# Kernel tuning notes

Hardware: AMD Instinct MI355X
Metric: run time of the kernel (lower is better)

Reference implementation:

```python
import jax, jax.numpy as jnp
import numpy as np
from jax import lax

DIM = 192
WS = (8, 8)
HEADS = 6
N = WS[0] * WS[1]
HEAD_DIM = DIM // HEADS
SCALE = HEAD_DIM ** -0.5


def _relative_position_index():
    ch, cw = np.arange(WS[0]), np.arange(WS[1])
    coords = np.stack(np.meshgrid(ch, cw, indexing='ij'))  # (2, Wh, Ww)
    cf = coords.reshape(2, -1)                              # (2, N)
    rel = cf[:, :, None] - cf[:, None, :]                   # (2, N, N)
    rel = rel.transpose(1, 2, 0).copy()
    rel[:, :, 0] += WS[0] - 1
    rel[:, :, 1] += WS[1] - 1
    rel[:, :, 0] *= 2 * WS[1] - 1
    return rel.sum(-1).astype(np.int32)                     # (N, N)


def setup_inputs() -> dict:
    key = jax.random.key(0)
    ks = jax.random.split(key, 8)
    B_ = 2048
    C3 = 3 * DIM
    x = jax.random.normal(ks[0], (B_, N, DIM), dtype=jnp.float32)
    mask = jnp.zeros((64, N, N), dtype=jnp.float32)  # (nW, N, N), 0/-inf mask; zeros here
    qkv_w = jax.random.normal(ks[1], (C3, DIM), dtype=jnp.float32) * 0.02   # 1x1 conv weight
    qkv_b = jnp.zeros((C3,), dtype=jnp.float32)
    dw_w = jax.random.normal(ks[2], (C3, 1, 3, 3), dtype=jnp.float32) * 0.1  # depthwise OIHW
    dw_b = jnp.zeros((C3,), dtype=jnp.float32)
    rpb_table = jax.random.normal(ks[3], ((2 * WS[0] - 1) * (2 * WS[1] - 1), HEADS), dtype=jnp.float32) * 0.02
    rel_idx = jnp.asarray(_relative_position_index())
    proj_w = jax.random.normal(ks[4], (DIM, DIM), dtype=jnp.float32) * 0.02
    proj_b = jnp.zeros((DIM,), dtype=jnp.float32)
    return {"x": x, "mask": mask, "qkv_w": qkv_w, "qkv_b": qkv_b, "dw_w": dw_w,
            "dw_b": dw_b, "rpb_table": rpb_table, "rel_idx": rel_idx,
            "proj_w": proj_w, "proj_b": proj_b}


def reference(x, mask, qkv_w, qkv_b, dw_w, dw_b, rpb_table, rel_idx, proj_w, proj_b):
    B_, n, C = x.shape
    C3 = 3 * C
    # 1x1 conv over channel dim (input treated as unbatched (C, B_, N) image)
    t = jnp.einsum('bnc,oc->bno', x, qkv_w) + qkv_b            # (B_, N, 3C)
    # depthwise 3x3 conv over the (B_, N) "spatial" grid, per the torch code
    t4 = t.transpose(2, 0, 1)[None]                            # (1, 3C, B_, N)
    t4 = lax.conv_general_dilated(
        t4, dw_w, window_strides=(1, 1), padding='SAME',
        feature_group_count=C3,
        dimension_numbers=('NCHW', 'OIHW', 'NCHW'))
    temp = (t4[0] + dw_b[:, None, None]).transpose(1, 2, 0)    # (B_, N, 3C)
    qkv = temp.reshape(B_, n, 3, HEADS, HEAD_DIM).transpose(2, 0, 3, 1, 4)
    q, k, v = qkv[0] * SCALE, qkv[1], qkv[2]                   # (B_, H, N, d)
    attn = jnp.einsum('bhnd,bhmd->bhnm', q, k)                 # (B_, H, N, N)
    bias = rpb_table[rel_idx.reshape(-1)].reshape(n, n, HEADS).transpose(2, 0, 1)
    attn = attn + bias[None]
    nW = mask.shape[0]
    attn = attn.reshape(B_ // nW, nW, HEADS, n, n) + mask[None, :, None]
    attn = jax.nn.softmax(attn.reshape(B_, HEADS, n, n), axis=-1)
    out = jnp.einsum('bhnm,bhmd->bhnd', attn, v)               # (B_, H, N, d)
    out = out.transpose(0, 2, 1, 3).reshape(B_, n, C)
    return out @ proj_w.T + proj_b
```

## Files before the change

kernel.cpp:

```cpp
#include <hip/hip_runtime.h>

#define NWIN 2048
#define NPOS 64
#define DIM  192
#define C3   576
#define HEADS 6
#define HD   32
#define MTOT (NWIN*NPOS)
#define SCALE 0.17677669529663687f

typedef __bf16 b16x8 __attribute__((ext_vector_type(8)));
typedef __bf16 b16x4 __attribute__((ext_vector_type(4)));
typedef float  f32x4 __attribute__((ext_vector_type(4)));

__device__ __forceinline__ b16x8 ld8(const float* p) {
    const f32x4 f0 = *(const f32x4*)p;
    const f32x4 f1 = *(const f32x4*)(p + 4);
    b16x8 r;
    r[0] = (__bf16)f0[0]; r[1] = (__bf16)f0[1]; r[2] = (__bf16)f0[2]; r[3] = (__bf16)f0[3];
    r[4] = (__bf16)f1[0]; r[5] = (__bf16)f1[1]; r[6] = (__bf16)f1[2]; r[7] = (__bf16)f1[3];
    return r;
}
__device__ __forceinline__ b16x8 ld8(const __bf16* p) { return *(const b16x8*)p; }

#define GTM 128
#define GTN 64
#define GLD 72

template <typename TA, typename TC>
__global__ __launch_bounds__(256, 3)
void gemm_bt(const TA* __restrict__ A, const float* __restrict__ W,
             const float* __restrict__ bias, TC* __restrict__ C, int N)
{
    __shared__ __bf16 As[GTM][GLD];
    __shared__ __bf16 Ws[GTN][GLD];
    const int ntiles = N / GTN;
    const int cpx = gridDim.x >> 3;
    const int lb  = (blockIdx.x & 7) * cpx + (blockIdx.x >> 3);
    const int bm = lb / ntiles;
    const int bn = lb % ntiles;
    const long m0 = (long)bm * GTM;
    const int  n0 = bn * GTN;
    const int tid  = threadIdx.x;
    const int wave = tid >> 6, lane = tid & 63;
    const int lr = lane & 15, lq = lane >> 4;

    f32x4 acc[2][4];
#pragma unroll
    for (int i = 0; i < 2; i++)
#pragma unroll
        for (int j = 0; j < 4; j++) acc[i][j] = (f32x4){0.f, 0.f, 0.f, 0.f};

    for (int kc = 0; kc < 3; kc++) {
#pragma unroll
        for (int i = 0; i < 4; i++) {
            int idx = tid + i * 256;
            int r = idx >> 3, c = idx & 7;
            *(b16x8*)&As[r][c * 8] = ld8(A + (m0 + r) * 192 + kc * 64 + c * 8);
        }
#pragma unroll
        for (int i = 0; i < 2; i++) {
            int idx = tid + i * 256;
            int r = idx >> 3, c = idx & 7;
            *(b16x8*)&Ws[r][c * 8] = ld8(W + (long)(n0 + r) * 192 + kc * 64 + c * 8);
        }
        __syncthreads();
#pragma unroll
        for (int kt = 0; kt < 2; kt++) {
            const int k0 = kt * 32 + lq * 8;
            b16x8 a0 = *(const b16x8*)&As[wave * 32 + lr][k0];
            b16x8 a1 = *(const b16x8*)&As[wave * 32 + 16 + lr][k0];
            b16x8 b0 = *(const b16x8*)&Ws[lr][k0];
            b16x8 b1 = *(const b16x8*)&Ws[16 + lr][k0];
            b16x8 b2 = *(const b16x8*)&Ws[32 + lr][k0];
            b16x8 b3 = *(const b16x8*)&Ws[48 + lr][k0];
            acc[0][0] = __builtin_amdgcn_mfma_f32_16x16x32_bf16(a0, b0, acc[0][0], 0, 0, 0);
            acc[0][1] = __builtin_amdgcn_mfma_f32_16x16x32_bf16(a0, b1, acc[0][1], 0, 0, 0);
            acc[0][2] = __builtin_amdgcn_mfma_f32_16x16x32_bf16(a0, b2, acc[0][2], 0, 0, 0);
            acc[0][3] = __builtin_amdgcn_mfma_f32_16x16x32_bf16(a0, b3, acc[0][3], 0, 0, 0);
            acc[1][0] = __builtin_amdgcn_mfma_f32_16x16x32_bf16(a1, b0, acc[1][0], 0, 0, 0);
            acc[1][1] = __builtin_amdgcn_mfma_f32_16x16x32_bf16(a1, b1, acc[1][1], 0, 0, 0);
            acc[1][2] = __builtin_amdgcn_mfma_f32_16x16x32_bf16(a1, b2, acc[1][2], 0, 0, 0);
            acc[1][3] = __builtin_amdgcn_mfma_f32_16x16x32_bf16(a1, b3, acc[1][3], 0, 0, 0);
        }
        __syncthreads();
    }
#pragma unroll
    for (int tn = 0; tn < 4; tn++) {
        float bv = bias[n0 + tn * 16 + lr];
#pragma unroll
        for (int tm = 0; tm < 2; tm++) {
#pragma unroll
            for (int r = 0; r < 4; r++) {
                long row = m0 + wave * 32 + tm * 16 + lq * 4 + r;
                C[row * N + (n0 + tn * 16 + lr)] = (TC)(acc[tm][tn][r] + bv);
            }
        }
    }
}

__global__ __launch_bounds__(576)
void dwconv(const __bf16* __restrict__ t, const float* __restrict__ dw_w,
            const float* __restrict__ dw_b, __bf16* __restrict__ u)
{
    const int tid = threadIdx.x;
    const int cg  = tid % 144;
    const int mr  = tid / 144;
    const int c0  = cg * 4;

    float w[9][4], bias[4];
#pragma unroll
    for (int e = 0; e < 4; e++) {
        bias[e] = dw_b[c0 + e];
#pragma unroll
        for (int tp = 0; tp < 9; tp++) w[tp][e] = dw_w[(c0 + e) * 9 + tp];
    }
    const float sc = (c0 < DIM) ? SCALE : 1.0f;

    const int b = blockIdx.x;
    const bool up = (b > 0), dn = (b < NWIN - 1);
    const __bf16* tb = t + (long)b * NPOS * C3 + c0;
    __bf16*       ub = u + (long)b * NPOS * C3 + c0;

    for (int i = 0; i < 16; i++) {
        const int n = i * 4 + mr;
        float acc[4] = {bias[0], bias[1], bias[2], bias[3]};
#pragma unroll
        for (int kh = 0; kh < 3; kh++) {
            if ((kh == 0 && !up) || (kh == 2 && !dn)) continue;
            const __bf16* rp = tb + (long)(kh - 1) * NPOS * C3 + (long)n * C3;
#pragma unroll
            for (int kw = 0; kw < 3; kw++) {
                const int nn = n + kw - 1;
                if (nn < 0 || nn >= NPOS) continue;
                b16x4 v = *(const b16x4*)(rp + (kw - 1) * C3);
#pragma unroll
                for (int e = 0; e < 4; e++) acc[e] += (float)v[e] * w[kh * 3 + kw][e];
            }
        }
        b16x4 o;
#pragma unroll
        for (int e = 0; e < 4; e++) o[e] = (__bf16)(acc[e] * sc);
        *(b16x4*)(ub + (long)n * C3) = o;
    }
}

#define P0v2 0
#define VT0  4608

__global__ __launch_bounds__(64, 3)
void attn_mfma(const __bf16* __restrict__ u, const float* __restrict__ mask,
               const float* __restrict__ rpb, __bf16* __restrict__ ctx)
{
    __shared__ __bf16 smem[4608 + 2304];
    __shared__ float  rpb_h[225];
    const int cpx = gridDim.x >> 3;
    const int lb  = (blockIdx.x & 7) * cpx + (blockIdx.x >> 3);
    const int b = lb / HEADS;
    const int h = lb % HEADS;
    const int lane = threadIdx.x;
    const int lr = lane & 15, lq = lane >> 4;

    for (int i = lane; i < 225; i += 64) rpb_h[i] = rpb[i * HEADS + h];

    const __bf16* ub = u + (long)b * NPOS * C3 + h * HD;

    {
        const __bf16* vp = ub + (long)lane * C3 + 2 * DIM;
        b16x8 v0 = *(const b16x8*)vp;
        b16x8 v1 = *(const b16x8*)(vp + 8);
        b16x8 v2 = *(const b16x8*)(vp + 16);
        b16x8 v3 = *(const b16x8*)(vp + 24);
#pragma unroll
        for (int e = 0; e < 8; e++) {
            smem[VT0 + (e     ) * 72 + lane] = v0[e];
            smem[VT0 + (e +  8) * 72 + lane] = v1[e];
            smem[VT0 + (e + 16) * 72 + lane] = v2[e];
            smem[VT0 + (e + 24) * 72 + lane] = v3[e];
        }
    }

    b16x8 aq[4], bk[4];
#pragma unroll
    for (int t4 = 0; t4 < 4; t4++) {
        aq[t4] = *(const b16x8*)(ub + (long)(t4 * 16 + lr) * C3 +       lq * 8);
        bk[t4] = *(const b16x8*)(ub + (long)(t4 * 16 + lr) * C3 + DIM + lq * 8);
    }

    f32x4 S[4][4];
#pragma unroll
    for (int tm = 0; tm < 4; tm++)
#pragma unroll
        for (int tn = 0; tn < 4; tn++) {
            S[tm][tn] = (f32x4){0.f, 0.f, 0.f, 0.f};
            S[tm][tn] = __builtin_amdgcn_mfma_f32_16x16x32_bf16(aq[tm], bk[tn], S[tm][tn], 0, 0, 0);
        }

    __syncthreads();

    const float* mbase = mask + (long)(b & 63) * 4096;
    float part[4][4];
#pragma unroll
    for (int tm = 0; tm < 4; tm++)
#pragma unroll
        for (int r = 0; r < 4; r++) part[tm][r] = 0.f;
#pragma unroll
    for (int tm = 0; tm < 4; tm++) {
#pragma unroll
        for (int r = 0; r < 4; r++) {
            const int row = tm * 16 + lq * 4 + r;
            const int rh = row >> 3, rw = row & 7;
#pragma unroll
            for (int tn = 0; tn < 4; tn++) {
                const int col = tn * 16 + lr;
                const int ridx = (rh - (col >> 3) + 7) * 15 + (rw - (col & 7) + 7);
                float sv = S[tm][tn][r] + rpb_h[ridx] + mbase[row * 64 + col];
                float ee = __expf(sv);
                part[tm][r] += ee;
                smem[P0v2 + row * 72 + col] = (__bf16)ee;
            }
        }
    }
#pragma unroll
    for (int st = 1; st < 16; st <<= 1)
#pragma unroll
        for (int tm = 0; tm < 4; tm++)
#pragma unroll
            for (int r = 0; r < 4; r++) part[tm][r] += __shfl_xor(part[tm][r], st);
    float inv[4][4];
#pragma unroll
    for (int tm = 0; tm < 4; tm++)
#pragma unroll
        for (int r = 0; r < 4; r++) inv[tm][r] = 1.0f / part[tm][r];

    __syncthreads();

    f32x4 O[4][2];
#pragma unroll
    for (int tm = 0; tm < 4; tm++)
#pragma unroll
        for (int tn2 = 0; tn2 < 2; tn2++) O[tm][tn2] = (f32x4){0.f, 0.f, 0.f, 0.f};
#pragma unroll
    for (int tk = 0; tk < 2; tk++) {
        b16x8 bv[2];
#pragma unroll
        for (int tn2 = 0; tn2 < 2; tn2++)
            bv[tn2] = *(const b16x8*)&smem[VT0 + (tn2 * 16 + lr) * 72 + tk * 32 + lq * 8];
#pragma unroll
        for (int tm = 0; tm < 4; tm++) {
            b16x8 ap = *(const b16x8*)&smem[P0v2 + (tm * 16 + lr) * 72 + tk * 32 + lq * 8];
#pragma unroll
            for (int tn2 = 0; tn2 < 2; tn2++)
                O[tm][tn2] = __builtin_amdgcn_mfma_f32_16x16x32_bf16(ap, bv[tn2], O[tm][tn2], 0, 0, 0);
        }
    }

#pragma unroll
    for (int tm = 0; tm < 4; tm++)
#pragma unroll
        for (int tn2 = 0; tn2 < 2; tn2++)
#pragma unroll
            for (int r = 0; r < 4; r++) {
                const int row = tm * 16 + lq * 4 + r;
                ctx[(long)(b * NPOS + row) * DIM + h * HD + tn2 * 16 + lr] =
                    (__bf16)(O[tm][tn2][r] * inv[tm][r]);
            }
}

#define Q0 0
#define K0 2560
#define P0 0
#define V0 5120

__global__ __launch_bounds__(64, 4)
void attn_fused(const __bf16* __restrict__ t, const float* __restrict__ dw_w,
                const float* __restrict__ dw_b, const float* __restrict__ mask,
                const float* __restrict__ rpb, __bf16* __restrict__ ctx)
{
    __shared__ __bf16 smem[7424];
    __shared__ float  rpb_h[225];
    const int bid = blockIdx.x;
    const int h   = bid >> 11;
    const int s_  = bid & 2047;
    const int b   = (s_ & 7) * 256 + (s_ >> 3);
    const int lane = threadIdx.x;
    const int lr = lane & 15, lq = lane >> 4;

    for (int i = lane; i < 225; i += 64) rpb_h[i] = rpb[i * HEADS + h];

    {
        const int kv = lane >> 5, d = lane & 31;
        const int o  = 192 + kv * 192 + h * 32 + d;
        float w[9];
#pragma unroll
        for (int tap = 0; tap < 9; tap++) w[tap] = dw_w[o * 9 + tap];
        const float cb = dw_b[o];
        const bool up = (b > 0), dn = (b < NWIN - 1);
        const __bf16* r1 = t + (long)b * NPOS * C3 + o;
        const __bf16* r0 = r1 - (long)NPOS * C3;
        const __bf16* r2 = r1 + (long)NPOS * C3;
        float p0 = 0.f, c0 = up ? (float)r0[0] : 0.f;
        float p1 = 0.f, c1 = (float)r1[0];
        float p2 = 0.f, c2 = dn ? (float)r2[0] : 0.f;
        const int base = kv ? (V0 + d * 72) : (K0 + d);
        const int step = kv ? 1 : 40;
        for (int nn = 0; nn < 64; nn++) {
            float n0 = 0.f, n1 = 0.f, n2 = 0.f;
            if (nn < 63) {
                const long off = (long)(nn + 1) * C3;
                if (up) n0 = (float)r0[off];
                n1 = (float)r1[off];
                if (dn) n2 = (float)r2[off];
            }
            float out = cb
                + w[0] * p0 + w[1] * c0 + w[2] * n0
                + w[3] * p1 + w[4] * c1 + w[5] * n1
                + w[6] * p2 + w[7] * c2 + w[8] * n2;
            smem[base + nn * step] = (__bf16)out;
            p0 = c0; c0 = n0; p1 = c1; c1 = n1; p2 = c2; c2 = n2;
        }
    }

    {
        float q[HD];
#pragma unroll
        for (int d = 0; d < HD; d++) q[d] = dw_b[h * HD + d];
#pragma unroll
        for (int kh = 0; kh < 3; kh++) {
            const int bb = b + kh - 1;
            if (bb < 0 || bb >= NWIN) continue;
#pragma unroll
            for (int kw = 0; kw < 3; kw++) {
                const int nn = lane + kw - 1;
                if (nn >= 0 && nn < NPOS) {
                    const b16x8* p = (const b16x8*)(t + (long)(bb * NPOS + nn) * C3 + h * HD);
#pragma unroll
                    for (int j = 0; j < 4; j++) {
                        b16x8 vv = p[j];
#pragma unroll
                        for (int e = 0; e < 8; e++)
                            q[j * 8 + e] += (float)vv[e] * dw_w[(h * HD + j * 8 + e) * 9 + kh * 3 + kw];
                    }
                }
            }
        }
#pragma unroll
        for (int d = 0; d < HD; d++) smem[Q0 + lane * 40 + d] = (__bf16)(q[d] * SCALE);
    }

    __syncthreads();

    b16x8 aq[4], bk[4];
#pragma unroll
    for (int tm = 0; tm < 4; tm++) aq[tm] = *(const b16x8*)&smem[Q0 + (tm * 16 + lr) * 40 + lq * 8];
#pragma unroll
    for (int tn = 0; tn < 4; tn++) bk[tn] = *(const b16x8*)&smem[K0 + (tn * 16 + lr) * 40 + lq * 8];
    f32x4 S[4][4];
#pragma unroll
    for (int tm = 0; tm < 4; tm++)
#pragma unroll
        for (int tn = 0; tn < 4; tn++) {
            S[tm][tn] = (f32x4){0.f, 0.f, 0.f, 0.f};
            S[tm][tn] = __builtin_amdgcn_mfma_f32_16x16x32_bf16(aq[tm], bk[tn], S[tm][tn], 0, 0, 0);
        }

    __syncthreads();

    const float* mbase = mask + (long)(b & 63) * 4096;
    float part[4][4];
#pragma unroll
    for (int tm = 0; tm < 4; tm++)
#pragma unroll
        for (int r = 0; r < 4; r++) part[tm][r] = 0.f;
#pragma unroll
    for (int tm = 0; tm < 4; tm++) {
#pragma unroll
        for (int r = 0; r < 4; r++) {
            const int row = tm * 16 + lq * 4 + r;
            const int rh = row >> 3, rw = row & 7;
#pragma unroll
            for (int tn = 0; tn < 4; tn++) {
                const int col = tn * 16 + lr;
                const int ridx = (rh - (col >> 3) + 7) * 15 + (rw - (col & 7) + 7);
                float sv = S[tm][tn][r] + rpb_h[ridx] + mbase[row * 64 + col];
                float ee = __expf(sv);
                part[tm][r] += ee;
                smem[P0 + row * 72 + col] = (__bf16)ee;
            }
        }
    }
#pragma unroll
    for (int st = 1; st < 16; st <<= 1)
#pragma unroll
        for (int tm = 0; tm < 4; tm++)
#pragma unroll
            for (int r = 0; r < 4; r++) part[tm][r] += __shfl_xor(part[tm][r], st);
    float inv[4][4];
#pragma unroll
    for (int tm = 0; tm < 4; tm++)
#pragma unroll
        for (int r = 0; r < 4; r++) inv[tm][r] = 1.0f / part[tm][r];

    __syncthreads();

    f32x4 O[4][2];
#pragma unroll
    for (int tm = 0; tm < 4; tm++)
#pragma unroll
        for (int tn2 = 0; tn2 < 2; tn2++) O[tm][tn2] = (f32x4){0.f, 0.f, 0.f, 0.f};
#pragma unroll
    for (int tk = 0; tk < 2; tk++) {
        b16x8 bv[2];
#pragma unroll
        for (int tn2 = 0; tn2 < 2; tn2++)
            bv[tn2] = *(const b16x8*)&smem[V0 + (tn2 * 16 + lr) * 72 + tk * 32 + lq * 8];
#pragma unroll
        for (int tm = 0; tm < 4; tm++) {
            b16x8 ap = *(const b16x8*)&smem[P0 + (tm * 16 + lr) * 72 + tk * 32 + lq * 8];
#pragma unroll
            for (int tn2 = 0; tn2 < 2; tn2++)
                O[tm][tn2] = __builtin_amdgcn_mfma_f32_16x16x32_bf16(ap, bv[tn2], O[tm][tn2], 0, 0, 0);
        }
    }

#pragma unroll
    for (int tm = 0; tm < 4; tm++)
#pragma unroll
        for (int tn2 = 0; tn2 < 2; tn2++)
#pragma unroll
            for (int r = 0; r < 4; r++) {
                const int row = tm * 16 + lq * 4 + r;
                ctx[(long)(b * NPOS + row) * DIM + h * HD + tn2 * 16 + lr] =
                    (__bf16)(O[tm][tn2][r] * inv[tm][r]);
            }
}

extern "C" void kernel_launch(void* const* d_in, const int* in_sizes, int n_in,
                              void* d_out, int out_size, void* d_ws, size_t ws_size,
                              hipStream_t stream)
{
    (void)in_sizes; (void)n_in; (void)out_size;
    const float* x      = (const float*)d_in[0];
    const float* mask   = (const float*)d_in[1];
    const float* qkv_w  = (const float*)d_in[2];
    const float* qkv_b  = (const float*)d_in[3];
    const float* dw_w   = (const float*)d_in[4];
    const float* dw_b   = (const float*)d_in[5];
    const float* rpb    = (const float*)d_in[6];
    const float* proj_w = (const float*)d_in[8];
    const float* proj_b = (const float*)d_in[9];
    float* out = (float*)d_out;

    __bf16* t = (__bf16*)d_ws;
    const size_t need = ((size_t)MTOT * C3 * 2 + (size_t)MTOT * DIM) * sizeof(__bf16);
    __bf16* ctx;

    gemm_bt<float, __bf16><<<(MTOT / GTM) * (C3 / GTN), 256, 0, stream>>>(x, qkv_w, qkv_b, t, C3);

    if (ws_size >= need) {
        __bf16* u = t + (size_t)MTOT * C3;
        ctx = u + (size_t)MTOT * C3;
        dwconv<<<NWIN, 576, 0, stream>>>(t, dw_w, dw_b, u);
        attn_mfma<<<NWIN * HEADS, 64, 0, stream>>>(u, mask, rpb, ctx);
    } else {
        ctx = t + (size_t)MTOT * C3;
        attn_fused<<<NWIN * HEADS, 64, 0, stream>>>(t, dw_w, dw_b, mask, rpb, ctx);
    }

    gemm_bt<__bf16, float><<<(MTOT / GTM) * (DIM / GTN), 256, 0, stream>>>(ctx, proj_w, proj_b, out, DIM);
}
```

Measured before the change: 592.8 us.

## Restructure depthwise conv with sliding-window register reuse and channel-split blocks

The depthwise 3x3 conv kernel now splits each window into three channel-group blocks of 192 threads, and each thread walks 16 consecutive positions. Neighbouring columns are kept in registers as a sliding window, so each row element is loaded once per thread instead of three times. The scale is folded into the weights and bias, and blocks are reordered in an XCD-aware way. The risk is lower parallelism per block and serial dependence across the 16-position walk.

```diff
diff --git a/kernel.cpp b/kernel.cpp
--- a/kernel.cpp
+++ b/kernel.cpp
@@ -99,49 +99,81 @@
     }
 }
 
-__global__ __launch_bounds__(576)
+__device__ __forceinline__ void ld4f(float* d, const __bf16* p) {
+    b16x4 v = *(const b16x4*)p;
+    d[0] = (float)v[0]; d[1] = (float)v[1]; d[2] = (float)v[2]; d[3] = (float)v[3];
+}
+
+__global__ __launch_bounds__(192)
 void dwconv(const __bf16* __restrict__ t, const float* __restrict__ dw_w,
             const float* __restrict__ dw_b, __bf16* __restrict__ u)
 {
     const int tid = threadIdx.x;
-    const int cg  = tid % 144;
-    const int mr  = tid / 144;
-    const int c0  = cg * 4;
-
-    float w[9][4], bias[4];
+    const int cg  = tid % 48;
+    const int mr  = tid / 48;
+    const int cpx = gridDim.x >> 3;
+    const int lb  = (blockIdx.x & 7) * cpx + (blockIdx.x >> 3);
+    const int b   = lb / 3;
+    const int gq  = lb % 3;
+    const int ch0 = gq * 192 + cg * 4;
+
+    const float sc = (ch0 < DIM) ? SCALE : 1.0f;
+    float w[9][4], bs[4];
 #pragma unroll
     for (int e = 0; e < 4; e++) {
-        bias[e] = dw_b[c0 + e];
-#pragma unroll
-        for (int tp = 0; tp < 9; tp++) w[tp][e] = dw_w[(c0 + e) * 9 + tp];
-    }
-    const float sc = (c0 < DIM) ? SCALE : 1.0f;
-
-    const int b = blockIdx.x;
+        bs[e] = dw_b[ch0 + e] * sc;
+#pragma unroll
+        for (int tp = 0; tp < 9; tp++) w[tp][e] = dw_w[(ch0 + e) * 9 + tp] * sc;
+    }
+
     const bool up = (b > 0), dn = (b < NWIN - 1);
-    const __bf16* tb = t + (long)b * NPOS * C3 + c0;
-    __bf16*       ub = u + (long)b * NPOS * C3 + c0;
-
-    for (int i = 0; i < 16; i++) {
-        const int n = i * 4 + mr;
-        float acc[4] = {bias[0], bias[1], bias[2], bias[3]};
-#pragma unroll
-        for (int kh = 0; kh < 3; kh++) {
-            if ((kh == 0 && !up) || (kh == 2 && !dn)) continue;
-            const __bf16* rp = tb + (long)(kh - 1) * NPOS * C3 + (long)n * C3;
-#pragma unroll
-            for (int kw = 0; kw < 3; kw++) {
-                const int nn = n + kw - 1;
-                if (nn < 0 || nn >= NPOS) continue;
-                b16x4 v = *(const b16x4*)(rp + (kw - 1) * C3);
-#pragma unroll
-                for (int e = 0; e < 4; e++) acc[e] += (float)v[e] * w[kh * 3 + kw][e];
-            }
+    const __bf16* r0 = t + ((long)(b - 1) * NPOS) * C3 + ch0;
+    const __bf16* r1 = t + ((long)b       * NPOS) * C3 + ch0;
+    const __bf16* r2 = t + ((long)(b + 1) * NPOS) * C3 + ch0;
+    const int n0 = mr * 16;
+    __bf16* ub = u + ((long)b * NPOS + n0) * C3 + ch0;
+
+    float p0[4] = {0,0,0,0}, p1[4] = {0,0,0,0}, p2[4] = {0,0,0,0};
+    float c0[4] = {0,0,0,0}, c1[4] = {0,0,0,0}, c2[4] = {0,0,0,0};
+    if (n0 > 0) {
+        const long off = (long)(n0 - 1) * C3;
+        if (up) ld4f(p0, r0 + off);
+        ld4f(p1, r1 + off);
+        if (dn) ld4f(p2, r2 + off);
+    }
+    {
+        const long off = (long)n0 * C3;
+        if (up) ld4f(c0, r0 + off);
+        ld4f(c1, r1 + off);
+        if (dn) ld4f(c2, r2 + off);
+    }
+
+#pragma unroll 4
+    for (int j = 0; j < 16; j++) {
+        const int n = n0 + j;
+        float x0[4] = {0,0,0,0}, x1[4] = {0,0,0,0}, x2[4] = {0,0,0,0};
+        if (n < 63) {
+            const long off = (long)(n + 1) * C3;
+            if (up) ld4f(x0, r0 + off);
+            ld4f(x1, r1 + off);
+            if (dn) ld4f(x2, r2 + off);
         }
         b16x4 o;
 #pragma unroll
-        for (int e = 0; e < 4; e++) o[e] = (__bf16)(acc[e] * sc);
-        *(b16x4*)(ub + (long)n * C3) = o;
+        for (int e = 0; e < 4; e++) {
+            float a = bs[e]
+                + w[0][e] * p0[e] + w[1][e] * c0[e] + w[2][e] * x0[e]
+                + w[3][e] * p1[e] + w[4][e] * c1[e] + w[5][e] * x1[e]
+                + w[6][e] * p2[e] + w[7][e] * c2[e] + w[8][e] * x2[e];
+            o[e] = (__bf16)a;
+        }
+        *(b16x4*)(ub + (long)j * C3) = o;
+#pragma unroll
+        for (int e = 0; e < 4; e++) {
+            p0[e] = c0[e]; c0[e] = x0[e];
+            p1[e] = c1[e]; c1[e] = x1[e];
+            p2[e] = c2[e]; c2[e] = x2[e];
+        }
     }
 }
 
@@ -460,7 +492,7 @@
     if (ws_size >= need) {
         __bf16* u = t + (size_t)MTOT * C3;
         ctx = u + (size_t)MTOT * C3;
-        dwconv<<<NWIN, 576, 0, stream>>>(t, dw_w, dw_b, u);
+        dwconv<<<NWIN * 3, 192, 0, stream>>>(t, dw_w, dw_b, u);
         attn_mfma<<<NWIN * HEADS, 64, 0, stream>>>(u, mask, rpb, ctx);
     } else {
         ctx = t + (size_t)MTOT * C3;
```

Result: faster. 541.1 us (-8.7%).
